# Optimization experiments

Measured on AMD Instinct MI355X. Metric: run time of the kernel, lower is better.

Reference implementation:

```python
import jax, jax.numpy as jnp
import numpy as np

NUM_SPEAKERS = 8  # static speaker vocabulary size for the per-speaker state


def setup_inputs() -> dict:
    key = jax.random.key(0)
    ks = jax.random.split(key, 6)
    B, T, L, D = 8, 256, 64, 768
    input_ids = jax.random.randint(ks[0], (B, T, L), 0, 32000, dtype=jnp.int32)
    speaker_ids = jax.random.randint(ks[1], (B, T), 0, NUM_SPEAKERS, dtype=jnp.int32)
    token_embeddings = jax.random.normal(ks[2], (B, T, L, D), dtype=jnp.float32)
    edu_embeddings = jax.random.normal(ks[3], (B, T, D), dtype=jnp.float32)
    # nn.Linear(d, d, bias=False) weights, torch layout [out, in]
    Wk = jax.random.normal(ks[4], (D, D), dtype=jnp.float32) / np.sqrt(D)
    Wv = jax.random.normal(ks[5], (D, D), dtype=jnp.float32) / np.sqrt(D)
    return {"input_ids": input_ids, "speaker_ids": speaker_ids,
            "token_embeddings": token_embeddings, "edu_embeddings": edu_embeddings,
            "Wk": Wk, "Wv": Wv}


def reference(input_ids, speaker_ids, token_embeddings, edu_embeddings, Wk, Wv):
    B, T, L = input_ids.shape
    D = edu_embeddings.shape[-1]
    # projections (torch Linear: x @ W.T)
    k = jnp.einsum('btd,ed->bte', edu_embeddings, Wk)  # [B,T,D]
    v = jnp.einsum('btd,ed->bte', edu_embeddings, Wv)  # [B,T,D]

    b_idx = jnp.arange(B)

    def step(state, inp):
        # state: per-speaker running kv_sum, [B, S, D, D]
        k_t, v_t, spk_t, tok_t = inp  # [B,D], [B,D], [B], [B,L,D]
        kv = k_t[:, :, None] * v_t[:, None, :]           # outer(k, v): [B,D,D]
        state = state.at[b_idx, spk_t].add(kv)           # segmented accumulate
        M = state[b_idx, spk_t]                          # [B,D,D] current speaker memory
        out_t = tok_t + jnp.einsum('bij,blj->bli', M, tok_t)
        return state, out_t

    state0 = jnp.zeros((B, NUM_SPEAKERS, D, D), dtype=token_embeddings.dtype)
    xs = (jnp.swapaxes(k, 0, 1), jnp.swapaxes(v, 0, 1),
          jnp.swapaxes(speaker_ids, 0, 1), jnp.swapaxes(token_embeddings, 0, 1))
    _, out = jax.lax.scan(step, state0, xs)              # out: [T,B,L,D]
    return jnp.swapaxes(out, 0, 1)                       # [B,T,L,D]
```

## Files before the change

### kernel.cpp

```cpp
#include <hip/hip_runtime.h>
#include <hip/hip_bf16.h>

#define NB 8
#define NT 256
#define NL 64
#define ND 768

typedef __attribute__((ext_vector_type(4))) float f32x4;
typedef __attribute__((ext_vector_type(8))) short bf16x8;

__device__ __forceinline__ short f2bs(float f) {
    __hip_bfloat16 h = __float2bfloat16(f);
    return *reinterpret_cast<short*>(&h);
}
__device__ __forceinline__ unsigned pack2(float a, float b) {
    return (unsigned)(ushort)f2bs(a) | ((unsigned)(ushort)f2bs(b) << 16);
}

__global__ __launch_bounds__(256, 4) void projm_kernel(
    const float* __restrict__ E, const float* __restrict__ Wk,
    const float* __restrict__ Wv, float* __restrict__ kws,
    float* __restrict__ vws)
{
    const float* W = (blockIdx.z == 0) ? Wk : Wv;
    float* O       = (blockIdx.z == 0) ? kws : vws;
    const int m0 = blockIdx.x * 64;
    const int e0 = blockIdx.y * 64;

    __shared__ ushort Et[2][4096];
    __shared__ ushort Wt[2][4096];

    const int tid = threadIdx.x;
    const int lane = tid & 63, w = tid >> 6;
    const int fr = lane & 15;
    const int fq = lane >> 4;
    const int row2 = tid >> 4;
    const int c4   = tid & 15;

    const f32x4 z4 = {0.f, 0.f, 0.f, 0.f};
    f32x4 acc[4];
    #pragma unroll
    for (int et = 0; et < 4; ++et) acc[et] = z4;

    float4 ea[2][4], wa[2][4];
    #pragma unroll
    for (int p = 0; p < 4; ++p) {
        ea[0][p] = *(const float4*)(E + (size_t)(m0 + row2 + 16 * p) * ND + c4 * 4);
        wa[0][p] = *(const float4*)(W + (size_t)(e0 + row2 + 16 * p) * ND + c4 * 4);
    }

    #pragma unroll
    for (int dt = 0; dt < 12; ++dt) {
        const int cur = dt & 1, nxt = cur ^ 1;
        #pragma unroll
        for (int p = 0; p < 4; ++p) {
            const int r = row2 + 16 * p;
            const int uidx = (r * 64 + c4 * 4) ^ ((r & 7) << 3);
            uint2 te; te.x = pack2(ea[cur][p].x, ea[cur][p].y); te.y = pack2(ea[cur][p].z, ea[cur][p].w);
            uint2 tw; tw.x = pack2(wa[cur][p].x, wa[cur][p].y); tw.y = pack2(wa[cur][p].z, wa[cur][p].w);
            *(uint2*)&Et[cur][uidx] = te;
            *(uint2*)&Wt[cur][uidx] = tw;
        }
        if (dt < 11) {
            const int c0 = (dt + 1) * 64 + c4 * 4;
            #pragma unroll
            for (int p = 0; p < 4; ++p) {
                ea[nxt][p] = *(const float4*)(E + (size_t)(m0 + row2 + 16 * p) * ND + c0);
                wa[nxt][p] = *(const float4*)(W + (size_t)(e0 + row2 + 16 * p) * ND + c0);
            }
        }
        __syncthreads();
        const int brow = w * 16 + fr;
        const int bsw  = (brow & 7) << 3;
        #pragma unroll
        for (int ks = 0; ks < 2; ++ks) {
            bf16x8 bv = *(const bf16x8*)&Et[cur][(brow * 64 + ks * 32 + fq * 8) ^ bsw];
            #pragma unroll
            for (int et = 0; et < 4; ++et) {
                const int arow = et * 16 + fr;
                bf16x8 af = *(const bf16x8*)&Wt[cur][(arow * 64 + ks * 32 + fq * 8) ^ ((arow & 7) << 3)];
                acc[et] = __builtin_amdgcn_mfma_f32_16x16x32_bf16(af, bv, acc[et], 0, 0, 0);
            }
        }
    }

    float* ob = O + (size_t)(m0 + w * 16 + fr) * ND + e0 + fq * 4;
    #pragma unroll
    for (int et = 0; et < 4; ++et)
        *(f32x4*)(ob + et * 16) = acc[et];
}

__global__ __launch_bounds__(256, 3) void fused_kernel(
    const int* __restrict__ spk, const float* __restrict__ tok,
    const float* __restrict__ kws, const float* __restrict__ vws,
    float* __restrict__ out)
{
    __shared__ int mlist[NT];
    __shared__ int wavecnt[4];
    __shared__ ushort U[8192];
    __shared__ ushort Vt[2][4096];
    __shared__ ushort Sb[4096];

    ushort* At0 = U;
    ushort* At1 = U + 4096;
    ushort* kT  = U;

    const int bt  = blockIdx.x;
    const int b   = bt >> 8;
    const int t   = bt & 255;
    const int tid = threadIdx.x;

    const int tgt = spk[b * NT + t];
    int my = -1;
    if (tid <= t) my = spk[b * NT + tid];
    const bool match = (tid <= t) && (my == tgt);
    unsigned long long bal = __ballot(match);
    const int lane = tid & 63, w = tid >> 6;
    if (lane == 0) wavecnt[w] = __popcll(bal);
    __syncthreads();
    int off = 0;
    #pragma unroll
    for (int ww = 0; ww < 4; ++ww) if (ww < w) off += wavecnt[ww];
    const int n = wavecnt[0] + wavecnt[1] + wavecnt[2] + wavecnt[3];
    const int before = __popcll(bal & ((1ull << lane) - 1ull));
    if (match) mlist[off + before] = tid;
    __syncthreads();

    const int fr = lane & 15;
    const int fq = lane >> 4;
    const int rb = tid >> 4;
    const int c4 = tid & 15;
    const int jr = tid >> 2;
    const int q  = tid & 3;

    const size_t tokbase = (size_t)bt * NL * ND;
    const float* vbase = vws + (size_t)b * NT * ND;
    const float* kbase = kws + (size_t)b * NT * ND;
    const f32x4 z4 = {0.f, 0.f, 0.f, 0.f};

    const int nchunk = min((n + 63) >> 6, 4);
    for (int cc = 0; cc < nchunk; ++cc) {
        const int j0 = cc * 64;

        int gr[4];
        #pragma unroll
        for (int p = 0; p < 4; ++p) {
            const int jj = j0 + rb + 16 * p;
            gr[p] = mlist[jj < n ? jj : n - 1];
        }
        float4 ta[4], va[4];
        #pragma unroll
        for (int p = 0; p < 4; ++p) {
            ta[p] = *(const float4*)(tok + tokbase + (size_t)(rb + 16 * p) * ND + c4 * 4);
            va[p] = *(const float4*)(vbase + (size_t)gr[p] * ND + c4 * 4);
        }
        f32x4 accS[4];
        #pragma unroll
        for (int jt = 0; jt < 4; ++jt) accS[jt] = z4;

        for (int dt = 0; dt < 12; ++dt) {
            const int cur = dt & 1;
            ushort* Atc = cur ? At1 : At0;
            #pragma unroll
            for (int p = 0; p < 4; ++p) {
                const int row = rb + 16 * p;
                const int uidx = (row * 64 + c4 * 4) ^ ((row & 7) << 3);
                uint2 tw; tw.x = pack2(ta[p].x, ta[p].y); tw.y = pack2(ta[p].z, ta[p].w);
                uint2 vw; vw.x = pack2(va[p].x, va[p].y); vw.y = pack2(va[p].z, va[p].w);
                *(uint2*)&Atc[uidx] = tw;
                *(uint2*)&Vt[cur][uidx] = vw;
            }
            if (dt < 11) {
                const int c0 = (dt + 1) * 64 + c4 * 4;
                #pragma unroll
                for (int p = 0; p < 4; ++p) {
                    ta[p] = *(const float4*)(tok + tokbase + (size_t)(rb + 16 * p) * ND + c0);
                    va[p] = *(const float4*)(vbase + (size_t)gr[p] * ND + c0);
                }
            }
            __syncthreads();
            const int arow = w * 16 + fr;
            #pragma unroll
            for (int ks = 0; ks < 2; ++ks) {
                bf16x8 af = *(const bf16x8*)&Atc[(arow * 64 + ks * 32 + fq * 8) ^ ((arow & 7) << 3)];
                #pragma unroll
                for (int jt = 0; jt < 4; ++jt) {
                    const int brow = jt * 16 + fr;
                    bf16x8 bv = *(const bf16x8*)&Vt[cur][(brow * 64 + ks * 32 + fq * 8) ^ ((brow & 7) << 3)];
                    accS[jt] = __builtin_amdgcn_mfma_f32_16x16x32_bf16(af, bv, accS[jt], 0, 0, 0);
                }
            }
        }

        #pragma unroll
        for (int jt = 0; jt < 4; ++jt) {
            #pragma unroll
            for (int i = 0; i < 4; ++i) {
                const int r = w * 16 + fq * 4 + i;
                const int c = jt * 16 + fr;
                Sb[(r * 64 + c) ^ ((r & 7) << 3)] = (ushort)f2bs(accS[jt][i]);
            }
        }
        __syncthreads();

        const int jj = j0 + jr;
        const int g = (jj < n) ? mlist[jj] : -1;
        const float* bp = (cc == 0) ? (tok + tokbase) : (const float*)(out + tokbase);
        const f32x4 zf = {0.f, 0.f, 0.f, 0.f};

        f32x4 kreg[8];
        #pragma unroll
        for (int p = 0; p < 8; ++p)
            kreg[p] = (g >= 0)
                ? *(const f32x4*)(kbase + (size_t)g * ND + (q + 4 * p) * 4)
                : zf;

        for (int st = 0; st < 6; ++st) {
            if (st > 0) __syncthreads();
            #pragma unroll
            for (int p = 0; p < 8; ++p) {
                #pragma unroll
                for (int e = 0; e < 4; ++e) {
                    const int dc = (q + 4 * p) * 4 + e;
                    kT[(dc * 64 + jr) ^ ((dc & 7) << 3)] = (ushort)f2bs(kreg[p][e]);
                }
            }
            f32x4 acco[8];
            {
                const float* rbp = bp + (size_t)(w * 16 + fr) * ND + st * 128 + fq * 4;
                #pragma unroll
                for (int ct = 0; ct < 8; ++ct)
                    acco[ct] = *(const f32x4*)(rbp + ct * 16);
            }
            if (st < 5) {
                const int c0 = (st + 1) * 128;
                #pragma unroll
                for (int p = 0; p < 8; ++p)
                    kreg[p] = (g >= 0)
                        ? *(const f32x4*)(kbase + (size_t)g * ND + c0 + (q + 4 * p) * 4)
                        : zf;
            }
            __syncthreads();

            const int srow = w * 16 + fr;
            const int ssw  = (srow & 7) << 3;
            #pragma unroll
            for (int ks = 0; ks < 2; ++ks) {
                bf16x8 bv = *(const bf16x8*)&Sb[(srow * 64 + ks * 32 + fq * 8) ^ ssw];
                #pragma unroll
                for (int ct = 0; ct < 8; ++ct) {
                    const int drow = ct * 16 + fr;
                    bf16x8 af = *(const bf16x8*)&kT[(drow * 64 + ks * 32 + fq * 8) ^ ((drow & 7) << 3)];
                    acco[ct] = __builtin_amdgcn_mfma_f32_16x16x32_bf16(af, bv, acco[ct], 0, 0, 0);
                }
            }
            float* ob = out + tokbase + (size_t)(w * 16 + fr) * ND + st * 128 + fq * 4;
            #pragma unroll
            for (int ct = 0; ct < 8; ++ct)
                *(f32x4*)(ob + ct * 16) = acco[ct];
        }
        __syncthreads();
    }
}

extern "C" void kernel_launch(void* const* d_in, const int* in_sizes, int n_in,
                              void* d_out, int out_size, void* d_ws, size_t ws_size,
                              hipStream_t stream) {
    const int*   spk = (const int*)d_in[1];
    const float* tok = (const float*)d_in[2];
    const float* edu = (const float*)d_in[3];
    const float* Wk  = (const float*)d_in[4];
    const float* Wv  = (const float*)d_in[5];

    const size_t kv_floats = (size_t)NB * NT * ND;
    float* kws = (float*)d_ws;
    float* vws = kws + kv_floats;
    float* outp = (float*)d_out;

    projm_kernel<<<dim3(2048 / 64, ND / 64, 2), 256, 0, stream>>>(edu, Wk, Wv, kws, vws);
    fused_kernel<<<NB * NT, 256, 0, stream>>>(spk, tok, kws, vws, outp);
}
```

Before: 315.8 us.

## Load token A-operand directly into registers, drop shared staging, raise occupancy

The token tile no longer goes through shared memory. Each wave loads its own MFMA A fragments from global memory into registers (double-buffered) and converts them to bf16 in place. This removes the LDS writes and reads for that operand, frees a 16KB shared buffer (V now reuses the union region), and raises the launch-bounds occupancy hint from 3 to 5. In exchange, each dt iteration now needs a second barrier to protect the single V double buffer, and the global loads are less coalesced per-lane 32-byte reads.

After: 594.9 us. +88.4%, slower.

```diff
diff --git a/kernel.cpp b/kernel.cpp
--- a/kernel.cpp
+++ b/kernel.cpp
@@ -15,6 +15,12 @@
 }
 __device__ __forceinline__ unsigned pack2(float a, float b) {
     return (unsigned)(ushort)f2bs(a) | ((unsigned)(ushort)f2bs(b) << 16);
+}
+__device__ __forceinline__ bf16x8 cvt8(float4 x, float4 y) {
+    bf16x8 r;
+    r[0] = f2bs(x.x); r[1] = f2bs(x.y); r[2] = f2bs(x.z); r[3] = f2bs(x.w);
+    r[4] = f2bs(y.x); r[5] = f2bs(y.y); r[6] = f2bs(y.z); r[7] = f2bs(y.w);
+    return r;
 }
 
 __global__ __launch_bounds__(256, 4) void projm_kernel(
@@ -90,7 +96,7 @@
         *(f32x4*)(ob + et * 16) = acc[et];
 }
 
-__global__ __launch_bounds__(256, 3) void fused_kernel(
+__global__ __launch_bounds__(256, 5) void fused_kernel(
     const int* __restrict__ spk, const float* __restrict__ tok,
     const float* __restrict__ kws, const float* __restrict__ vws,
     float* __restrict__ out)
@@ -98,11 +104,10 @@
     __shared__ int mlist[NT];
     __shared__ int wavecnt[4];
     __shared__ ushort U[8192];
-    __shared__ ushort Vt[2][4096];
     __shared__ ushort Sb[4096];
 
-    ushort* At0 = U;
-    ushort* At1 = U + 4096;
+    ushort* Vt0 = U;
+    ushort* Vt1 = U + 4096;
     ushort* kT  = U;
 
     const int bt  = blockIdx.x;
@@ -136,6 +141,7 @@
     const size_t tokbase = (size_t)bt * NL * ND;
     const float* vbase = vws + (size_t)b * NT * ND;
     const float* kbase = kws + (size_t)b * NT * ND;
+    const float* tp = tok + tokbase + (size_t)(w * 16 + fr) * ND;
     const f32x4 z4 = {0.f, 0.f, 0.f, 0.f};
 
     const int nchunk = min((n + 63) >> 6, 4);
@@ -148,48 +154,56 @@
             const int jj = j0 + rb + 16 * p;
             gr[p] = mlist[jj < n ? jj : n - 1];
         }
-        float4 ta[4], va[4];
-        #pragma unroll
-        for (int p = 0; p < 4; ++p) {
-            ta[p] = *(const float4*)(tok + tokbase + (size_t)(rb + 16 * p) * ND + c4 * 4);
+        float4 va[4];
+        #pragma unroll
+        for (int p = 0; p < 4; ++p)
             va[p] = *(const float4*)(vbase + (size_t)gr[p] * ND + c4 * 4);
+        float4 aR[2][4];
+        #pragma unroll
+        for (int ks = 0; ks < 2; ++ks) {
+            aR[0][2 * ks]     = *(const float4*)(tp + ks * 32 + fq * 8);
+            aR[0][2 * ks + 1] = *(const float4*)(tp + ks * 32 + fq * 8 + 4);
         }
         f32x4 accS[4];
         #pragma unroll
         for (int jt = 0; jt < 4; ++jt) accS[jt] = z4;
 
         for (int dt = 0; dt < 12; ++dt) {
-            const int cur = dt & 1;
-            ushort* Atc = cur ? At1 : At0;
+            const int cur = dt & 1, nxt = cur ^ 1;
+            ushort* Vtc = cur ? Vt1 : Vt0;
             #pragma unroll
             for (int p = 0; p < 4; ++p) {
                 const int row = rb + 16 * p;
                 const int uidx = (row * 64 + c4 * 4) ^ ((row & 7) << 3);
-                uint2 tw; tw.x = pack2(ta[p].x, ta[p].y); tw.y = pack2(ta[p].z, ta[p].w);
                 uint2 vw; vw.x = pack2(va[p].x, va[p].y); vw.y = pack2(va[p].z, va[p].w);
-                *(uint2*)&Atc[uidx] = tw;
-                *(uint2*)&Vt[cur][uidx] = vw;
+                *(uint2*)&Vtc[uidx] = vw;
             }
             if (dt < 11) {
                 const int c0 = (dt + 1) * 64 + c4 * 4;
                 #pragma unroll
-                for (int p = 0; p < 4; ++p) {
-                    ta[p] = *(const float4*)(tok + tokbase + (size_t)(rb + 16 * p) * ND + c0);
+                for (int p = 0; p < 4; ++p)
                     va[p] = *(const float4*)(vbase + (size_t)gr[p] * ND + c0);
-                }
             }
             __syncthreads();
-            const int arow = w * 16 + fr;
+            if (dt < 11) {
+                const int c0 = (dt + 1) * 64;
+                #pragma unroll
+                for (int ks = 0; ks < 2; ++ks) {
+                    aR[nxt][2 * ks]     = *(const float4*)(tp + c0 + ks * 32 + fq * 8);
+                    aR[nxt][2 * ks + 1] = *(const float4*)(tp + c0 + ks * 32 + fq * 8 + 4);
+                }
+            }
             #pragma unroll
             for (int ks = 0; ks < 2; ++ks) {
-                bf16x8 af = *(const bf16x8*)&Atc[(arow * 64 + ks * 32 + fq * 8) ^ ((arow & 7) << 3)];
+                bf16x8 af = cvt8(aR[cur][2 * ks], aR[cur][2 * ks + 1]);
                 #pragma unroll
                 for (int jt = 0; jt < 4; ++jt) {
                     const int brow = jt * 16 + fr;
-                    bf16x8 bv = *(const bf16x8*)&Vt[cur][(brow * 64 + ks * 32 + fq * 8) ^ ((brow & 7) << 3)];
+                    bf16x8 bv = *(const bf16x8*)&Vtc[(brow * 64 + ks * 32 + fq * 8) ^ ((brow & 7) << 3)];
                     accS[jt] = __builtin_amdgcn_mfma_f32_16x16x32_bf16(af, bv, accS[jt], 0, 0, 0);
                 }
             }
+            __syncthreads();
         }
 
         #pragma unroll
@@ -206,14 +220,13 @@
         const int jj = j0 + jr;
         const int g = (jj < n) ? mlist[jj] : -1;
         const float* bp = (cc == 0) ? (tok + tokbase) : (const float*)(out + tokbase);
-        const f32x4 zf = {0.f, 0.f, 0.f, 0.f};
 
         f32x4 kreg[8];
         #pragma unroll
         for (int p = 0; p < 8; ++p)
             kreg[p] = (g >= 0)
                 ? *(const f32x4*)(kbase + (size_t)g * ND + (q + 4 * p) * 4)
-                : zf;
+                : z4;
 
         for (int st = 0; st < 6; ++st) {
             if (st > 0) __syncthreads();
@@ -238,7 +251,7 @@
                 for (int p = 0; p < 8; ++p)
                     kreg[p] = (g >= 0)
                         ? *(const f32x4*)(kbase + (size_t)g * ND + c0 + (q + 4 * p) * 4)
-                        : zf;
+                        : z4;
             }
             __syncthreads();
 
```
